# Optimization experiments

Measured on AMD Instinct MI355X. Metric: run time of the kernel, lower is better.

## Reference

```python
import jax, jax.numpy as jnp
import numpy as np

N_BUS = 300
N_GBUS = 69
N_LINE = 411
G_BUS0 = 1
VMAX = 1.06
VMIN = 0.94
L_LIMIT = 1.0
LG_MAX = (1.0, 1.0, 1.0)
BATCH = 32768


def setup_inputs() -> dict:
    key = jax.random.key(0)
    ks = jax.random.split(key, 18)
    f = lambda k, s: jax.random.normal(k, s, dtype=jnp.float32)
    return {
        "Volt": f(ks[0], (BATCH, 2 * N_BUS)),
        "P_Gens": f(ks[1], (BATCH, 2 * N_GBUS)),
        "P_Loads": f(ks[2], (BATCH, 2 * N_BUS)),
        "n_o_l_p": f(ks[3], (BATCH, 2 * N_BUS)),
        "n_o_mu_g_u": f(ks[4], (BATCH, 2 * N_GBUS)),
        "n_o_mu_g_d": f(ks[5], (BATCH, 2 * N_GBUS)),
        "n_o_mu_v_u": f(ks[6], (BATCH, N_BUS)),
        "n_o_mu_v_d": f(ks[7], (BATCH, N_BUS)),
        "n_o_mu_i_u": f(ks[8], (BATCH, N_LINE)),
        "Y": f(ks[9], (2 * N_BUS, 2 * N_BUS)) * 0.1,
        "Yconj": f(ks[10], (2 * N_BUS, 2 * N_BUS)) * 0.1,
        "Ybr": f(ks[11], (2 * N_LINE, 2 * N_LINE)) * 0.1,
        "IM": f(ks[12], (2 * N_LINE, 2 * N_BUS)) * 0.1,
        "Map_g": f(ks[13], (2 * N_GBUS, 2 * N_BUS)) * 0.1,
        "Map_L": f(ks[14], (2 * N_BUS, 2 * N_BUS)) * 0.1,
        "Gen_max": jax.random.uniform(ks[15], (1, 2 * N_GBUS), dtype=jnp.float32) + 0.5,
        "Gen_min": -jax.random.uniform(ks[16], (1, 2 * N_GBUS), dtype=jnp.float32) - 0.5,
        "C_Pg": f(ks[17], (1, N_GBUS)),
    }


def reference(Volt, P_Gens, P_Loads, n_o_l_p, n_o_mu_g_u, n_o_mu_g_d,
              n_o_mu_v_u, n_o_mu_v_d, n_o_mu_i_u,
              Y, Yconj, Ybr, IM, Map_g, Map_L, Gen_max, Gen_min, C_Pg):
    n = N_BUS
    B = Volt.shape[0]
    Bf = jnp.asarray(B, Volt.dtype)
    relu = jax.nn.relu

    Vre = Volt[:, :n]
    Vim = Volt[:, n:2 * n]

    # --- per-bus quadratic-form loop, vectorized ---------------------------
    # diag(Volt @ (M_i Y) @ Volt^T)[b] = Volt[b,i-1]*(Y[i-1]@Volt[b]) + Volt[b,n+i-1]*(Y[n+i-1]@Volt[b])
    quad_p = Volt * (Volt @ Y.T)      # [B, 2n]; quad_p[b,r] = Volt[b,r]*(Y[r]@Volt[b])
    quad_q = Volt * (Volt @ Yconj.T)  # [B, 2n]
    # TF broadcast quirk: [B] diag + [B,1] mismatch -> [B,B], reduce_sum(axis=1)
    # gives sum_j diag[j] (scalar) + B * mismatch[b].  Loop runs i = 1..n-1.
    scalar_pq = (jnp.sum(quad_p[:, 0:n - 1]) + jnp.sum(quad_p[:, n:2 * n - 1])
                 + jnp.sum(quad_q[:, 0:n - 1]) + jnp.sum(quad_q[:, n:2 * n - 1]))
    mism = P_Loads @ Map_L - P_Gens @ Map_g  # [B, 2n]
    mism_sum = jnp.sum(mism[:, 0:n - 1], axis=1) + jnp.sum(mism[:, n:2 * n - 1], axis=1)

    kkt = jnp.sum(jnp.abs(Volt[:, n + G_BUS0 - 1]))  # scalar seed
    kkt = kkt + scalar_pq + Bf * mism_sum            # -> [B]

    # --- inequality / complementarity terms --------------------------------
    kkt = kkt + jnp.sum(relu(P_Gens - Gen_max), axis=1)
    kkt = kkt + jnp.sum(relu(Gen_min - P_Gens), axis=1)

    v_up = Vre ** 2 + Vim ** 2 - VMAX ** 2
    v_dn = VMIN ** 2 - Vre ** 2 + Vim ** 2  # sign kept exactly as in original
    kkt = kkt + jnp.sum(relu(v_up), axis=1)
    kkt = kkt + jnp.sum(relu(v_dn), axis=1)

    Ibr = Volt @ IM.T @ Ybr.T  # == (Ybr @ (IM @ Volt^T))^T, [B, 2*n_line]
    i_up = Ibr[:, :N_LINE] ** 2 + Ibr[:, N_LINE:] ** 2 - L_LIMIT ** 2
    kkt = kkt + jnp.sum(relu(i_up), axis=1)

    kkt = kkt + jnp.sum(jnp.abs(n_o_mu_g_u * (P_Gens - Gen_max)), axis=1) / N_GBUS
    kkt = kkt + jnp.sum(jnp.abs(n_o_mu_g_d * (Gen_min - P_Gens)), axis=1) / N_GBUS
    kkt = kkt + jnp.sum(jnp.abs(n_o_mu_v_u * v_up), axis=1)
    kkt = kkt + jnp.sum(jnp.abs(n_o_mu_v_d * v_dn), axis=1)
    kkt = kkt + jnp.sum(jnp.abs(n_o_mu_i_u * i_up), axis=1)

    # --- stationarity w.r.t. generator injections ---------------------------
    C_Qg = jnp.zeros((1, N_GBUS), Volt.dtype)
    cost = jnp.concatenate([C_Pg, C_Qg], axis=1)  # [1, 2*n_gbus]
    stat = (n_o_mu_g_u * LG_MAX[1] - n_o_mu_g_d * LG_MAX[2]
            + (n_o_l_p * LG_MAX[0]) @ Map_g.T - cost)
    kkt = kkt + jnp.sum(jnp.abs(stat), axis=1)

    # --- dual feasibility ----------------------------------------------------
    kkt = kkt + jnp.sum(relu(-n_o_mu_g_u), axis=1)
    kkt = kkt + jnp.sum(relu(-n_o_mu_g_d), axis=1)
    kkt = kkt + jnp.sum(relu(-n_o_mu_v_u), axis=1)
    kkt = kkt + jnp.sum(relu(-n_o_mu_v_d), axis=1)
    kkt = kkt + jnp.sum(relu(-n_o_mu_i_u), axis=1)
    return kkt
```

## Files before the change

kernel.cpp:

```cpp
#include <hip/hip_runtime.h>

#define BATCH   32768
#define NLINE   411
#define NTILES  14
#define RTILES  256

typedef __attribute__((ext_vector_type(8))) short  short8;
typedef __attribute__((ext_vector_type(4))) float  f32x4;

#define WS_SCALAR   0
#define WS_KROWS    64
#define WS_MAPL     131136
#define WS_MAPG     133536
#define WS_ATMP     134144
#define WS_BMF      2106944
#define WS_VBF      4400704
#define WS_NEED_FAST (4400704 + 41943040)
#define WS_ZERO_BYTES 2106944

__device__ __forceinline__ unsigned short f2bf(float f) {
    unsigned int u = __float_as_uint(f);
    unsigned int r = (u + 0x7FFFu + ((u >> 16) & 1u)) >> 16;
    return (unsigned short)r;
}

#if defined(__has_builtin)
#  if __has_builtin(__builtin_amdgcn_cvt_pk_bf16_f32)
#    define HAVE_PK_BF16 1
#  endif
#endif

__device__ __forceinline__ unsigned int pk2bf(float a, float b) {
#ifdef HAVE_PK_BF16
    typedef __bf16 bf16x2 __attribute__((ext_vector_type(2)));
    bf16x2 r = __builtin_amdgcn_cvt_pk_bf16_f32(a, b);
    return __builtin_bit_cast(unsigned int, r);
#else
    return (unsigned int)f2bf(a) | ((unsigned int)f2bf(b) << 16);
#endif
}

__global__ void prep_colsums(const float* __restrict__ MapL, const float* __restrict__ Mapg,
                             float* __restrict__ mapL_s, float* __restrict__ mapg_s) {
    int w = threadIdx.x >> 6, lane = threadIdx.x & 63;
    int row = blockIdx.x * 4 + w;
    const float* src;
    float* dst;
    if (row < 600)      { src = MapL + (size_t)row * 600; dst = mapL_s + row; }
    else if (row < 738) { src = Mapg + (size_t)(row - 600) * 600; dst = mapg_s + (row - 600); }
    else return;
    float s = 0.f;
    for (int j = lane; j < 600; j += 64)
        if (j != 299 && j != 599) s += src[j];
    for (int m = 32; m >= 1; m >>= 1) s += __shfl_xor(s, m);
    if (lane == 0) *dst = s;
}

__global__ __launch_bounds__(256) void prep_A(const float* __restrict__ Ybr,
                                              const float* __restrict__ IM,
                                              float* __restrict__ Atmp) {
    int bid = blockIdx.x;
    int ks = bid & 3;
    int t2 = bid >> 2;
    int bc = t2 % 10, br = t2 / 10;
    int r0 = br * 64, c0 = bc * 64;
    int kb = ks * 206;
    int ke = (kb + 206 < 822) ? kb + 206 : 822;

    __shared__ float Yt[64][33];
    __shared__ float Xt[32][65];
    int t = threadIdx.x;
    int tx = t & 15, ty = t >> 4;
    float c[4][4] = {};

    for (int kk = kb; kk < ke; kk += 32) {
        __syncthreads();
        for (int e = t; e < 2048; e += 256) {
            int yr = e >> 5, yk = e & 31;
            int gr = r0 + yr, gk = kk + yk;
            Yt[yr][yk] = (gr < 822 && gk < ke) ? Ybr[(size_t)gr * 822 + gk] : 0.f;
        }
        for (int e = t; e < 2048; e += 256) {
            int xk = e >> 6, xc = e & 63;
            int gk = kk + xk, gc = c0 + xc;
            Xt[xk][xc] = (gk < ke && gc < 600) ? IM[(size_t)gk * 600 + gc] : 0.f;
        }
        __syncthreads();
        for (int k2 = 0; k2 < 32; ++k2) {
            float a[4], b[4];
#pragma unroll
            for (int ii = 0; ii < 4; ++ii) a[ii] = Yt[ty * 4 + ii][k2];
#pragma unroll
            for (int jj = 0; jj < 4; ++jj) b[jj] = Xt[k2][tx * 4 + jj];
#pragma unroll
            for (int ii = 0; ii < 4; ++ii)
#pragma unroll
                for (int jj = 0; jj < 4; ++jj) c[ii][jj] += a[ii] * b[jj];
        }
    }
#pragma unroll
    for (int ii = 0; ii < 4; ++ii)
#pragma unroll
        for (int jj = 0; jj < 4; ++jj) {
            int gr = r0 + ty * 4 + ii, gc = c0 + tx * 4 + jj;
            if (gr < 822 && gc < 600) atomicAdd(Atmp + (size_t)gr * 600 + gc, c[ii][jj]);
        }
}

__global__ void prep_packF(const float* __restrict__ Y, const float* __restrict__ Yconj,
                           const float* __restrict__ Mapg, const float* __restrict__ Atmp,
                           unsigned short* __restrict__ BmF) {
    int ntkc = blockIdx.x >> 2;
    int nt = ntkc / 10, kc = ntkc % 10;
    int S = (blockIdx.x & 3) * 256 + threadIdx.x;
    int ig = S >> 7, ks = (S >> 6) & 1, ln = S & 63;
    int rc = ig * 16 + (ln & 15);
    int kb = ks * 32 + ((ln >> 4) << 3);
    int n = nt * 128 + rc;
    unsigned short out[8];
#pragma unroll
    for (int j = 0; j < 8; ++j) {
        int k = kc * 64 + kb + j;
        float v = 0.f;
        if (k < 600) {
            if (n < 600) {
                if (n != 299 && n != 599)
                    v = Y[(size_t)n * 600 + k] + Yconj[(size_t)n * 600 + k];
            } else if (n >= 640 && n < 1536) {
                int idx = n - 640;
                int l = idx >> 1, h = idx & 1;
                if (l < NLINE) v = Atmp[(size_t)(h * NLINE + l) * 600 + k];
            } else if (n >= 1536) {
                int g = n - 1536;
                if (g < 138) v = Mapg[(size_t)g * 600 + k];
            }
        }
        out[j] = f2bf(v);
    }
    *(short8*)(BmF + (size_t)(ntkc * 1024 + S) * 8) = *(short8*)out;
}

__global__ __launch_bounds__(256) void prep_duties_conv(
    const float* __restrict__ Volt, const float* __restrict__ PL,
    const float* __restrict__ mu_vu, const float* __restrict__ mu_vd,
    const float* __restrict__ mapL_s, unsigned short* __restrict__ Vbf,
    float* __restrict__ kkt_rows, float* __restrict__ scalar_acc, int doConv) {
    __shared__ float mls[600];
    __shared__ float sred[4];
    int t = threadIdx.x;
    for (int j = t; j < 600; j += 256) mls[j] = mapL_s[j];
    __syncthreads();
    int w = t >> 6, lane = t & 63;
    int b = blockIdx.x * 4 + w;

    if (doConv) {
        for (int c = lane * 4; c < 600; c += 256) {
            f32x4 x = *(const f32x4*)(Volt + (size_t)b * 600 + c);
            uint2 p;
            p.x = pk2bf(x[0], x[1]);
            p.y = pk2bf(x[2], x[3]);
            *(uint2*)(Vbf + (size_t)b * 640 + c) = p;
        }
        if (lane < 10) {
            uint2 z = make_uint2(0u, 0u);
            *(uint2*)(Vbf + (size_t)b * 640 + 600 + lane * 4) = z;
        }
    }
    float s = 0.f;
    for (int j = lane; j < 300; j += 64) {
        float vr = Volt[(size_t)b * 600 + j];
        float vi = Volt[(size_t)b * 600 + 300 + j];
        float muu = mu_vu[(size_t)b * 300 + j];
        float mud = mu_vd[(size_t)b * 300 + j];
        float sq = vr * vr, si = vi * vi;
        float vu = sq + si - 1.1236f;
        float vd = 0.8836f - sq + si;
        s += fmaxf(vu, 0.f) + fmaxf(vd, 0.f) + fabsf(muu * vu) + fabsf(mud * vd)
           + fmaxf(-muu, 0.f) + fmaxf(-mud, 0.f);
    }
    float s2 = 0.f;
    for (int j = lane; j < 600; j += 64) s2 += PL[(size_t)b * 600 + j] * mls[j];
    s += 32768.0f * s2;
    for (int m = 32; m >= 1; m >>= 1) s += __shfl_xor(s, m);
    if (lane == 0) kkt_rows[b] = s;
    float v3 = (lane == 0) ? fabsf(Volt[(size_t)b * 600 + 300]) : 0.f;
    if (lane == 0) sred[w] = v3;
    __syncthreads();
    if (t == 0) atomicAdd(scalar_acc, sred[0] + sred[1] + sred[2] + sred[3]);
}

__global__ __launch_bounds__(256, 4) void kkt_main(
    const float* __restrict__ Volt, const float* __restrict__ nolp,
    const float* __restrict__ PG,
    const float* __restrict__ mu_gu, const float* __restrict__ mu_gd,
    const float* __restrict__ mu_iu,
    const float* __restrict__ Gmax, const float* __restrict__ Gmin,
    const float* __restrict__ CPg,
    const unsigned short* __restrict__ Vbf, const unsigned short* __restrict__ BmF,
    const float* __restrict__ mapg_s, float* __restrict__ kkt_rows,
    float* __restrict__ scalar_acc, int useVbf) {

    int idx = blockIdx.x;
    int xcd = idx & 7;
    int q = idx >> 3;
    int nt = q % NTILES;
    int rg = q / NTILES;
    int rt = rg * 8 + xcd;
    int b0 = rt * 128;

    int t = threadIdx.x;
    int lane = t & 63, w = t >> 6, wr = w >> 1, wc = w & 1;

    __shared__ short8 Asm[1024];
    __shared__ short8 Bsm[1024];
    __shared__ float  redbuf[4];

    bool fastA = (nt < 12) && useVbf;
    const float* Af32 = (nt < 12) ? Volt : nolp;

    int rcA[4], kbA[4];
#pragma unroll
    for (int m = 0; m < 4; ++m) {
        int S = m * 256 + t;
        int ig = S >> 7, ks = (S >> 6) & 1, ln = S & 63;
        rcA[m] = ig * 16 + (ln & 15);
        kbA[m] = ks * 32 + ((ln >> 4) << 3);
    }

    f32x4 acc[4][4] = {};

    for (int kc = 0; kc < 10; ++kc) {
        int k0 = kc * 64;
        __syncthreads();
        const unsigned short* bSrc = BmF + (size_t)(nt * 10 + kc) * 1024 * 8;
#pragma unroll
        for (int m = 0; m < 4; ++m) {
            int S = m * 256 + t;
            __builtin_amdgcn_global_load_lds(
                (const __attribute__((address_space(1))) unsigned int*)(bSrc + (size_t)S * 8),
                (__attribute__((address_space(3))) unsigned int*)&Bsm[S], 16, 0, 0);
        }
        if (fastA) {
#pragma unroll
            for (int m = 0; m < 4; ++m) {
                int S = m * 256 + t;
                __builtin_amdgcn_global_load_lds(
                    (const __attribute__((address_space(1))) unsigned int*)(Vbf + (size_t)(b0 + rcA[m]) * 640 + k0 + kbA[m]),
                    (__attribute__((address_space(3))) unsigned int*)&Asm[S], 16, 0, 0);
            }
        } else {
#pragma unroll
            for (int m = 0; m < 4; ++m) {
                int S = m * 256 + t;
                int gk = k0 + kbA[m];
                short8 av = (short8)0;
                if (gk < 600) {
                    const f32x4* p = (const f32x4*)(Af32 + (size_t)(b0 + rcA[m]) * 600 + gk);
                    f32x4 x0 = p[0], x1 = p[1];
                    uint2 a0, a1;
                    a0.x = pk2bf(x0[0], x0[1]); a0.y = pk2bf(x0[2], x0[3]);
                    a1.x = pk2bf(x1[0], x1[1]); a1.y = pk2bf(x1[2], x1[3]);
                    av = __builtin_bit_cast(short8, make_uint4(a0.x, a0.y, a1.x, a1.y));
                }
                Asm[S] = av;
            }
        }
        __syncthreads();
#pragma unroll
        for (int ks = 0; ks < 2; ++ks) {
            short8 af[4], bfr[4];
#pragma unroll
            for (int ii = 0; ii < 4; ++ii) af[ii] = Asm[((wr * 4 + ii) * 2 + ks) * 64 + lane];
#pragma unroll
            for (int jj = 0; jj < 4; ++jj) bfr[jj] = Bsm[((wc * 4 + jj) * 2 + ks) * 64 + lane];
#pragma unroll
            for (int ii = 0; ii < 4; ++ii)
#pragma unroll
                for (int jj = 0; jj < 4; ++jj)
                    acc[ii][jj] = __builtin_amdgcn_mfma_f32_16x16x32_bf16(af[ii], bfr[jj], acc[ii][jj], 0, 0, 0);
        }
    }

    if (nt < 5) {
        float qa = 0.f;
#pragma unroll
        for (int ii = 0; ii < 4; ++ii)
#pragma unroll
            for (int jj = 0; jj < 4; ++jj)
#pragma unroll
                for (int r2 = 0; r2 < 4; ++r2) {
                    int row = wr * 64 + ii * 16 + ((lane >> 4) << 2) + r2;
                    int col = nt * 128 + wc * 64 + jj * 16 + (lane & 15);
                    if (col < 600) {
                        float v = Volt[(size_t)(b0 + row) * 600 + col];
                        qa += acc[ii][jj][r2] * v;
                    }
                }
        for (int m = 32; m >= 1; m >>= 1) qa += __shfl_xor(qa, m);
        if (lane == 0) redbuf[w] = qa;
        __syncthreads();
        if (t == 0) atomicAdd(scalar_acc, redbuf[0] + redbuf[1] + redbuf[2] + redbuf[3]);
    } else if (nt < 12) {
        float racc[16];
#pragma unroll
        for (int s = 0; s < 16; ++s) racc[s] = 0.f;
#pragma unroll
        for (int ii = 0; ii < 4; ++ii)
#pragma unroll
            for (int jj = 0; jj < 4; ++jj)
#pragma unroll
                for (int r2 = 0; r2 < 4; ++r2) {
                    float u = acc[ii][jj][r2];
                    float up = __shfl_xor(u, 1);
                    int col = nt * 128 + wc * 64 + jj * 16 + (lane & 15);
                    int l = (col - 640) >> 1;
                    float contrib = 0.f;
                    if (l < NLINE && !(lane & 1)) {
                        int row = wr * 64 + ii * 16 + ((lane >> 4) << 2) + r2;
                        float iu = u * u + up * up - 1.0f;
                        float mu = mu_iu[(size_t)(b0 + row) * NLINE + l];
                        contrib = fmaxf(iu, 0.f) + fabsf(mu * iu) + fmaxf(-mu, 0.f);
                    }
                    racc[ii * 4 + r2] += contrib;
                }
#pragma unroll
        for (int s = 0; s < 16; ++s) {
            float v = racc[s];
            v += __shfl_xor(v, 1); v += __shfl_xor(v, 2);
            v += __shfl_xor(v, 4); v += __shfl_xor(v, 8);
            if ((lane & 15) == 0) {
                int row = wr * 64 + (s >> 2) * 16 + ((lane >> 4) << 2) + (s & 3);
                atomicAdd(kkt_rows + b0 + row, v);
            }
        }
    } else {
        float racc[16];
#pragma unroll
        for (int s = 0; s < 16; ++s) racc[s] = 0.f;
#pragma unroll
        for (int ii = 0; ii < 4; ++ii)
#pragma unroll
            for (int jj = 0; jj < 4; ++jj)
#pragma unroll
                for (int r2 = 0; r2 < 4; ++r2) {
                    int col = nt * 128 + wc * 64 + jj * 16 + (lane & 15);
                    int g = col - 1536;
                    float contrib = 0.f;
                    if (g < 138) {
                        int row = wr * 64 + ii * 16 + ((lane >> 4) << 2) + r2;
                        size_t ix = (size_t)(b0 + row) * 138 + g;
                        float u = acc[ii][jj][r2];
                        float gu = mu_gu[ix], gd = mu_gd[ix], pg = PG[ix];
                        float gmx = Gmax[g], gmn = Gmin[g];
                        float cst = (g < 69) ? CPg[g] : 0.f;
                        float t1 = pg - gmx, t2 = gmn - pg;
                        float st = u + gu - gd - cst;
                        contrib = fabsf(st) + fmaxf(t1, 0.f) + fmaxf(t2, 0.f)
                                + (fabsf(gu * t1) + fabsf(gd * t2)) * (1.0f / 69.0f)
                                + fmaxf(-gu, 0.f) + fmaxf(-gd, 0.f)
                                - 32768.0f * pg * mapg_s[g];
                    }
                    racc[ii * 4 + r2] += contrib;
                }
#pragma unroll
        for (int s = 0; s < 16; ++s) {
            float v = racc[s];
            v += __shfl_xor(v, 1); v += __shfl_xor(v, 2);
            v += __shfl_xor(v, 4); v += __shfl_xor(v, 8);
            if ((lane & 15) == 0) {
                int row = wr * 64 + (s >> 2) * 16 + ((lane >> 4) << 2) + (s & 3);
                atomicAdd(kkt_rows + b0 + row, v);
            }
        }
    }
}

__global__ void finalize_k(const float* __restrict__ kkt_rows, const float* __restrict__ scalar_acc,
                           float* __restrict__ out) {
    int i = blockIdx.x * 256 + threadIdx.x;
    out[i] = kkt_rows[i] + scalar_acc[0];
}

extern "C" void kernel_launch(void* const* d_in, const int* in_sizes, int n_in,
                              void* d_out, int out_size, void* d_ws, size_t ws_size,
                              hipStream_t stream) {
    const float* Volt  = (const float*)d_in[0];
    const float* PG    = (const float*)d_in[1];
    const float* PL    = (const float*)d_in[2];
    const float* nolp  = (const float*)d_in[3];
    const float* mu_gu = (const float*)d_in[4];
    const float* mu_gd = (const float*)d_in[5];
    const float* mu_vu = (const float*)d_in[6];
    const float* mu_vd = (const float*)d_in[7];
    const float* mu_iu = (const float*)d_in[8];
    const float* Y     = (const float*)d_in[9];
    const float* Yconj = (const float*)d_in[10];
    const float* Ybr   = (const float*)d_in[11];
    const float* IM    = (const float*)d_in[12];
    const float* Mapg  = (const float*)d_in[13];
    const float* MapL  = (const float*)d_in[14];
    const float* Gmax  = (const float*)d_in[15];
    const float* Gmin  = (const float*)d_in[16];
    const float* CPg   = (const float*)d_in[17];

    char* ws = (char*)d_ws;
    float* scalar_acc       = (float*)(ws + WS_SCALAR);
    float* kkt_rows         = (float*)(ws + WS_KROWS);
    float* mapLs            = (float*)(ws + WS_MAPL);
    float* mapgs            = (float*)(ws + WS_MAPG);
    float* Atmp             = (float*)(ws + WS_ATMP);
    unsigned short* BmF     = (unsigned short*)(ws + WS_BMF);
    unsigned short* Vbf     = (unsigned short*)(ws + WS_VBF);

    int useVbf = (ws_size >= (size_t)WS_NEED_FAST) ? 1 : 0;

    hipMemsetAsync(d_ws, 0, WS_ZERO_BYTES, stream);
    prep_colsums<<<185, 256, 0, stream>>>(MapL, Mapg, mapLs, mapgs);
    prep_A<<<520, 256, 0, stream>>>(Ybr, IM, Atmp);
    prep_packF<<<560, 256, 0, stream>>>(Y, Yconj, Mapg, Atmp, BmF);
    prep_duties_conv<<<8192, 256, 0, stream>>>(Volt, PL, mu_vu, mu_vd, mapLs,
                                               Vbf, kkt_rows, scalar_acc, useVbf);
    kkt_main<<<RTILES * NTILES, 256, 0, stream>>>(Volt, nolp, PG, mu_gu, mu_gd, mu_iu,
                                                  Gmax, Gmin, CPg, Vbf, BmF, mapgs,
                                                  kkt_rows, scalar_acc, useVbf);
    finalize_k<<<BATCH / 256, 256, 0, stream>>>(kkt_rows, scalar_acc, (float*)d_out);
}
```

Before: 789.0 us.

## Fuse prep into persistent row-block GEMM with A resident in LDS

Each 64-row block now converts its Volt (and later nolp) slab to bf16 once into LDS and sweeps all 14 column tiles, double-buffering B tiles via async global-to-LDS loads. The separate Volt-to-bf16 conversion kernel and the bf16 workspace copy are removed, and the per-row duty and load terms are folded into the first iterations of the main loop. This cuts repeated global reads of A across column tiles and one kernel launch. The cost is a large LDS footprint and one block per CU (512 blocks), so there is less latency hiding.

```diff
diff --git a/kernel.cpp b/kernel.cpp
--- a/kernel.cpp
+++ b/kernel.cpp
@@ -3,7 +3,9 @@
 #define BATCH   32768
 #define NLINE   411
 #define NTILES  14
-#define RTILES  256
+#define PAIRS   7
+#define ROWS    64
+#define NBLK    (BATCH / ROWS)
 
 typedef __attribute__((ext_vector_type(8))) short  short8;
 typedef __attribute__((ext_vector_type(4))) float  f32x4;
@@ -14,8 +16,6 @@
 #define WS_MAPG     133536
 #define WS_ATMP     134144
 #define WS_BMF      2106944
-#define WS_VBF      4400704
-#define WS_NEED_FAST (4400704 + 41943040)
 #define WS_ZERO_BYTES 2106944
 
 __device__ __forceinline__ unsigned short f2bf(float f) {
@@ -140,239 +140,244 @@
     *(short8*)(BmF + (size_t)(ntkc * 1024 + S) * 8) = *(short8*)out;
 }
 
-__global__ __launch_bounds__(256) void prep_duties_conv(
-    const float* __restrict__ Volt, const float* __restrict__ PL,
+__device__ __forceinline__ void stage_a(const float* __restrict__ src, int b0,
+                                        short8* Abuf, int t) {
+#pragma unroll
+    for (int h = 0; h < 2; ++h) {
+        f32x4 x[20];
+        int Sb = h * 2560;
+#pragma unroll
+        for (int m = 0; m < 10; ++m) {
+            int S = Sb + m * 256 + t;
+            int kc = S >> 9, r = S & 511;
+            int g = r >> 6, ln = r & 63;
+            int row = b0 + ((g >> 1) << 4) + (ln & 15);
+            int k = (kc << 6) + ((g & 1) << 5) + ((ln >> 4) << 3);
+            if (k < 600) {
+                const f32x4* p = (const f32x4*)(src + (size_t)row * 600 + k);
+                x[2 * m] = p[0]; x[2 * m + 1] = p[1];
+            } else {
+                f32x4 z = {0.f, 0.f, 0.f, 0.f};
+                x[2 * m] = z; x[2 * m + 1] = z;
+            }
+        }
+#pragma unroll
+        for (int m = 0; m < 10; ++m) {
+            int S = Sb + m * 256 + t;
+            f32x4 a = x[2 * m], b = x[2 * m + 1];
+            Abuf[S] = __builtin_bit_cast(short8,
+                make_uint4(pk2bf(a[0], a[1]), pk2bf(a[2], a[3]),
+                           pk2bf(b[0], b[1]), pk2bf(b[2], b[3])));
+        }
+    }
+}
+
+__device__ __forceinline__ void issue_b(const unsigned short* __restrict__ BmF,
+                                        int p, int kc, short8* dst, int t) {
+#pragma unroll
+    for (int m = 0; m < 8; ++m) {
+        int S = m * 256 + t;
+        int ntl2 = S >> 10, Sl = S & 1023;
+        const unsigned short* src = BmF +
+            (size_t)(((p * 2 + ntl2) * 10 + kc) * 1024 + Sl) * 8;
+        __builtin_amdgcn_global_load_lds(
+            (const __attribute__((address_space(1))) unsigned int*)src,
+            (__attribute__((address_space(3))) unsigned int*)(dst + S), 16, 0, 0);
+    }
+}
+
+__global__ __launch_bounds__(256, 1) void kkt_main(
+    const float* __restrict__ Volt, const float* __restrict__ nolp,
+    const float* __restrict__ PG, const float* __restrict__ PL,
+    const float* __restrict__ mu_gu, const float* __restrict__ mu_gd,
     const float* __restrict__ mu_vu, const float* __restrict__ mu_vd,
-    const float* __restrict__ mapL_s, unsigned short* __restrict__ Vbf,
-    float* __restrict__ kkt_rows, float* __restrict__ scalar_acc, int doConv) {
-    __shared__ float mls[600];
-    __shared__ float sred[4];
-    int t = threadIdx.x;
-    for (int j = t; j < 600; j += 256) mls[j] = mapL_s[j];
-    __syncthreads();
-    int w = t >> 6, lane = t & 63;
-    int b = blockIdx.x * 4 + w;
-
-    if (doConv) {
-        for (int c = lane * 4; c < 600; c += 256) {
-            f32x4 x = *(const f32x4*)(Volt + (size_t)b * 600 + c);
-            uint2 p;
-            p.x = pk2bf(x[0], x[1]);
-            p.y = pk2bf(x[2], x[3]);
-            *(uint2*)(Vbf + (size_t)b * 640 + c) = p;
-        }
-        if (lane < 10) {
-            uint2 z = make_uint2(0u, 0u);
-            *(uint2*)(Vbf + (size_t)b * 640 + 600 + lane * 4) = z;
-        }
-    }
-    float s = 0.f;
-    for (int j = lane; j < 300; j += 64) {
-        float vr = Volt[(size_t)b * 600 + j];
-        float vi = Volt[(size_t)b * 600 + 300 + j];
-        float muu = mu_vu[(size_t)b * 300 + j];
-        float mud = mu_vd[(size_t)b * 300 + j];
-        float sq = vr * vr, si = vi * vi;
-        float vu = sq + si - 1.1236f;
-        float vd = 0.8836f - sq + si;
-        s += fmaxf(vu, 0.f) + fmaxf(vd, 0.f) + fabsf(muu * vu) + fabsf(mud * vd)
-           + fmaxf(-muu, 0.f) + fmaxf(-mud, 0.f);
-    }
-    float s2 = 0.f;
-    for (int j = lane; j < 600; j += 64) s2 += PL[(size_t)b * 600 + j] * mls[j];
-    s += 32768.0f * s2;
-    for (int m = 32; m >= 1; m >>= 1) s += __shfl_xor(s, m);
-    if (lane == 0) kkt_rows[b] = s;
-    float v3 = (lane == 0) ? fabsf(Volt[(size_t)b * 600 + 300]) : 0.f;
-    if (lane == 0) sred[w] = v3;
-    __syncthreads();
-    if (t == 0) atomicAdd(scalar_acc, sred[0] + sred[1] + sred[2] + sred[3]);
-}
-
-__global__ __launch_bounds__(256, 4) void kkt_main(
-    const float* __restrict__ Volt, const float* __restrict__ nolp,
-    const float* __restrict__ PG,
-    const float* __restrict__ mu_gu, const float* __restrict__ mu_gd,
     const float* __restrict__ mu_iu,
     const float* __restrict__ Gmax, const float* __restrict__ Gmin,
     const float* __restrict__ CPg,
-    const unsigned short* __restrict__ Vbf, const unsigned short* __restrict__ BmF,
-    const float* __restrict__ mapg_s, float* __restrict__ kkt_rows,
-    float* __restrict__ scalar_acc, int useVbf) {
-
-    int idx = blockIdx.x;
-    int xcd = idx & 7;
-    int q = idx >> 3;
-    int nt = q % NTILES;
-    int rg = q / NTILES;
-    int rt = rg * 8 + xcd;
-    int b0 = rt * 128;
-
-    int t = threadIdx.x;
-    int lane = t & 63, w = t >> 6, wr = w >> 1, wc = w & 1;
-
-    __shared__ short8 Asm[1024];
-    __shared__ short8 Bsm[1024];
-    __shared__ float  redbuf[4];
-
-    bool fastA = (nt < 12) && useVbf;
-    const float* Af32 = (nt < 12) ? Volt : nolp;
-
-    int rcA[4], kbA[4];
-#pragma unroll
-    for (int m = 0; m < 4; ++m) {
-        int S = m * 256 + t;
-        int ig = S >> 7, ks = (S >> 6) & 1, ln = S & 63;
-        rcA[m] = ig * 16 + (ln & 15);
-        kbA[m] = ks * 32 + ((ln >> 4) << 3);
-    }
+    const unsigned short* __restrict__ BmF,
+    const float* __restrict__ mapLs, const float* __restrict__ mapgs,
+    float* __restrict__ kkt_rows, float* __restrict__ scalar_acc) {
+
+    __shared__ short8 Abuf[5120];
+    __shared__ short8 Bsm[2][2048];
+    __shared__ float  mls[600];
+    __shared__ float  sacc;
+
+    int t = threadIdx.x, lane = t & 63, w = t >> 6;
+    int b0 = blockIdx.x * ROWS;
+    int ntl = w >> 1, wc2 = w & 1;
+
+    if (t == 0) sacc = 0.f;
+    for (int j = t; j < 600; j += 256) mls[j] = mapLs[j];
+
+    stage_a(Volt, b0, Abuf, t);
+    issue_b(BmF, 0, 0, &Bsm[0][0], t);
+    __syncthreads();
 
     f32x4 acc[4][4] = {};
-
-    for (int kc = 0; kc < 10; ++kc) {
-        int k0 = kc * 64;
-        __syncthreads();
-        const unsigned short* bSrc = BmF + (size_t)(nt * 10 + kc) * 1024 * 8;
-#pragma unroll
-        for (int m = 0; m < 4; ++m) {
-            int S = m * 256 + t;
-            __builtin_amdgcn_global_load_lds(
-                (const __attribute__((address_space(1))) unsigned int*)(bSrc + (size_t)S * 8),
-                (__attribute__((address_space(3))) unsigned int*)&Bsm[S], 16, 0, 0);
-        }
-        if (fastA) {
-#pragma unroll
-            for (int m = 0; m < 4; ++m) {
-                int S = m * 256 + t;
-                __builtin_amdgcn_global_load_lds(
-                    (const __attribute__((address_space(1))) unsigned int*)(Vbf + (size_t)(b0 + rcA[m]) * 640 + k0 + kbA[m]),
-                    (__attribute__((address_space(3))) unsigned int*)&Asm[S], 16, 0, 0);
-            }
-        } else {
-#pragma unroll
-            for (int m = 0; m < 4; ++m) {
-                int S = m * 256 + t;
-                int gk = k0 + kbA[m];
-                short8 av = (short8)0;
-                if (gk < 600) {
-                    const f32x4* p = (const f32x4*)(Af32 + (size_t)(b0 + rcA[m]) * 600 + gk);
-                    f32x4 x0 = p[0], x1 = p[1];
-                    uint2 a0, a1;
-                    a0.x = pk2bf(x0[0], x0[1]); a0.y = pk2bf(x0[2], x0[3]);
-                    a1.x = pk2bf(x1[0], x1[1]); a1.y = pk2bf(x1[2], x1[3]);
-                    av = __builtin_bit_cast(short8, make_uint4(a0.x, a0.y, a1.x, a1.y));
-                }
-                Asm[S] = av;
-            }
-        }
-        __syncthreads();
+    float dscal = 0.f;
+
+    for (int s = 0; s < PAIRS * 10; ++s) {
+        int p = s / 10, kc = s % 10;
+
+        if (s == 60) {
+            stage_a(nolp, b0, Abuf, t);
+            __syncthreads();
+        }
+        int sn = s + 1;
+        if (sn < PAIRS * 10) issue_b(BmF, sn / 10, sn % 10, &Bsm[sn & 1][0], t);
+
+        const short8* Ak = Abuf + kc * 512;
+        const short8* Bp = &Bsm[s & 1][ntl * 1024];
 #pragma unroll
         for (int ks = 0; ks < 2; ++ks) {
             short8 af[4], bfr[4];
 #pragma unroll
-            for (int ii = 0; ii < 4; ++ii) af[ii] = Asm[((wr * 4 + ii) * 2 + ks) * 64 + lane];
-#pragma unroll
-            for (int jj = 0; jj < 4; ++jj) bfr[jj] = Bsm[((wc * 4 + jj) * 2 + ks) * 64 + lane];
+            for (int ii = 0; ii < 4; ++ii) af[ii] = Ak[(((ii << 1) | ks) << 6) + lane];
+#pragma unroll
+            for (int jj = 0; jj < 4; ++jj)
+                bfr[jj] = Bp[(((((wc2 << 2) | jj) << 1) | ks) << 6) + lane];
 #pragma unroll
             for (int ii = 0; ii < 4; ++ii)
 #pragma unroll
                 for (int jj = 0; jj < 4; ++jj)
                     acc[ii][jj] = __builtin_amdgcn_mfma_f32_16x16x32_bf16(af[ii], bfr[jj], acc[ii][jj], 0, 0, 0);
         }
-    }
-
-    if (nt < 5) {
-        float qa = 0.f;
-#pragma unroll
-        for (int ii = 0; ii < 4; ++ii)
-#pragma unroll
-            for (int jj = 0; jj < 4; ++jj)
-#pragma unroll
-                for (int r2 = 0; r2 < 4; ++r2) {
-                    int row = wr * 64 + ii * 16 + ((lane >> 4) << 2) + r2;
-                    int col = nt * 128 + wc * 64 + jj * 16 + (lane & 15);
-                    if (col < 600) {
-                        float v = Volt[(size_t)(b0 + row) * 600 + col];
-                        qa += acc[ii][jj][r2] * v;
+
+        if (s < 16) {
+            int r = b0 + s * 4 + w;
+            const float* vrow = Volt + (size_t)r * 600;
+            float sd = 0.f;
+            for (int j = lane; j < 300; j += 64) {
+                float vr = vrow[j], vi = vrow[300 + j];
+                float muu = mu_vu[(size_t)r * 300 + j];
+                float mud = mu_vd[(size_t)r * 300 + j];
+                float sq = vr * vr, si = vi * vi;
+                float vu = sq + si - 1.1236f;
+                float vd = 0.8836f - sq + si;
+                sd += fmaxf(vu, 0.f) + fmaxf(vd, 0.f) + fabsf(muu * vu) + fabsf(mud * vd)
+                    + fmaxf(-muu, 0.f) + fmaxf(-mud, 0.f);
+            }
+            float s2 = 0.f;
+            for (int j = lane; j < 600; j += 64) s2 += PL[(size_t)r * 600 + j] * mls[j];
+            sd += 32768.0f * s2;
+            for (int m = 32; m >= 1; m >>= 1) sd += __shfl_xor(sd, m);
+            if (lane == 0) {
+                atomicAdd(kkt_rows + r, sd);
+                dscal += fabsf(vrow[300]);
+            }
+        }
+
+        if (kc == 9) {
+            int cb = p * 4 + w;
+            int c0 = cb * 64;
+            if (cb < 10) {
+                float qa = 0.f;
+#pragma unroll
+                for (int ii = 0; ii < 4; ++ii)
+#pragma unroll
+                    for (int jj = 0; jj < 4; ++jj) {
+                        int col = c0 + jj * 16 + (lane & 15);
+                        if (col < 600) {
+#pragma unroll
+                            for (int r2 = 0; r2 < 4; ++r2) {
+                                int row = ii * 16 + ((lane >> 4) << 2) + r2;
+                                qa += acc[ii][jj][r2] * Volt[(size_t)(b0 + row) * 600 + col];
+                            }
+                        }
+                    }
+                for (int m = 32; m >= 1; m >>= 1) qa += __shfl_xor(qa, m);
+                if (lane == 0) atomicAdd(&sacc, qa);
+            } else if (cb < 24) {
+                float racc[16];
+#pragma unroll
+                for (int q2 = 0; q2 < 16; ++q2) racc[q2] = 0.f;
+#pragma unroll
+                for (int ii = 0; ii < 4; ++ii)
+#pragma unroll
+                    for (int jj = 0; jj < 4; ++jj) {
+                        int col = c0 + jj * 16 + (lane & 15);
+                        int l = (col - 640) >> 1;
+#pragma unroll
+                        for (int r2 = 0; r2 < 4; ++r2) {
+                            float u = acc[ii][jj][r2];
+                            float up = __shfl_xor(u, 1);
+                            float contrib = 0.f;
+                            if (l < NLINE && !(lane & 1)) {
+                                int row = ii * 16 + ((lane >> 4) << 2) + r2;
+                                float iu = u * u + up * up - 1.0f;
+                                float mu = mu_iu[(size_t)(b0 + row) * NLINE + l];
+                                contrib = fmaxf(iu, 0.f) + fabsf(mu * iu) + fmaxf(-mu, 0.f);
+                            }
+                            racc[ii * 4 + r2] += contrib;
+                        }
+                    }
+#pragma unroll
+                for (int q2 = 0; q2 < 16; ++q2) {
+                    float v = racc[q2];
+                    v += __shfl_xor(v, 1); v += __shfl_xor(v, 2);
+                    v += __shfl_xor(v, 4); v += __shfl_xor(v, 8);
+                    if ((lane & 15) == 0) {
+                        int row = (q2 >> 2) * 16 + ((lane >> 4) << 2) + (q2 & 3);
+                        atomicAdd(kkt_rows + b0 + row, v);
                     }
                 }
-        for (int m = 32; m >= 1; m >>= 1) qa += __shfl_xor(qa, m);
-        if (lane == 0) redbuf[w] = qa;
+            } else {
+                float racc[16];
+#pragma unroll
+                for (int q2 = 0; q2 < 16; ++q2) racc[q2] = 0.f;
+#pragma unroll
+                for (int ii = 0; ii < 4; ++ii)
+#pragma unroll
+                    for (int jj = 0; jj < 4; ++jj) {
+                        int col = c0 + jj * 16 + (lane & 15);
+                        int g = col - 1536;
+#pragma unroll
+                        for (int r2 = 0; r2 < 4; ++r2) {
+                            float contrib = 0.f;
+                            if (g < 138) {
+                                int row = ii * 16 + ((lane >> 4) << 2) + r2;
+                                size_t ix = (size_t)(b0 + row) * 138 + g;
+                                float u = acc[ii][jj][r2];
+                                float gu = mu_gu[ix], gd = mu_gd[ix], pg = PG[ix];
+                                float gmx = Gmax[g], gmn = Gmin[g];
+                                float cst = (g < 69) ? CPg[g] : 0.f;
+                                float t1 = pg - gmx, t2 = gmn - pg;
+                                float st = u + gu - gd - cst;
+                                contrib = fabsf(st) + fmaxf(t1, 0.f) + fmaxf(t2, 0.f)
+                                        + (fabsf(gu * t1) + fabsf(gd * t2)) * (1.0f / 69.0f)
+                                        + fmaxf(-gu, 0.f) + fmaxf(-gd, 0.f)
+                                        - 32768.0f * pg * mapgs[g];
+                            }
+                            racc[ii * 4 + r2] += contrib;
+                        }
+                    }
+#pragma unroll
+                for (int q2 = 0; q2 < 16; ++q2) {
+                    float v = racc[q2];
+                    v += __shfl_xor(v, 1); v += __shfl_xor(v, 2);
+                    v += __shfl_xor(v, 4); v += __shfl_xor(v, 8);
+                    if ((lane & 15) == 0) {
+                        int row = (q2 >> 2) * 16 + ((lane >> 4) << 2) + (q2 & 3);
+                        atomicAdd(kkt_rows + b0 + row, v);
+                    }
+                }
+            }
+#pragma unroll
+            for (int ii = 0; ii < 4; ++ii)
+#pragma unroll
+                for (int jj = 0; jj < 4; ++jj) {
+                    f32x4 z = {0.f, 0.f, 0.f, 0.f};
+                    acc[ii][jj] = z;
+                }
+        }
+
         __syncthreads();
-        if (t == 0) atomicAdd(scalar_acc, redbuf[0] + redbuf[1] + redbuf[2] + redbuf[3]);
-    } else if (nt < 12) {
-        float racc[16];
-#pragma unroll
-        for (int s = 0; s < 16; ++s) racc[s] = 0.f;
-#pragma unroll
-        for (int ii = 0; ii < 4; ++ii)
-#pragma unroll
-            for (int jj = 0; jj < 4; ++jj)
-#pragma unroll
-                for (int r2 = 0; r2 < 4; ++r2) {
-                    float u = acc[ii][jj][r2];
-                    float up = __shfl_xor(u, 1);
-                    int col = nt * 128 + wc * 64 + jj * 16 + (lane & 15);
-                    int l = (col - 640) >> 1;
-                    float contrib = 0.f;
-                    if (l < NLINE && !(lane & 1)) {
-                        int row = wr * 64 + ii * 16 + ((lane >> 4) << 2) + r2;
-                        float iu = u * u + up * up - 1.0f;
-                        float mu = mu_iu[(size_t)(b0 + row) * NLINE + l];
-                        contrib = fmaxf(iu, 0.f) + fabsf(mu * iu) + fmaxf(-mu, 0.f);
-                    }
-                    racc[ii * 4 + r2] += contrib;
-                }
-#pragma unroll
-        for (int s = 0; s < 16; ++s) {
-            float v = racc[s];
-            v += __shfl_xor(v, 1); v += __shfl_xor(v, 2);
-            v += __shfl_xor(v, 4); v += __shfl_xor(v, 8);
-            if ((lane & 15) == 0) {
-                int row = wr * 64 + (s >> 2) * 16 + ((lane >> 4) << 2) + (s & 3);
-                atomicAdd(kkt_rows + b0 + row, v);
-            }
-        }
-    } else {
-        float racc[16];
-#pragma unroll
-        for (int s = 0; s < 16; ++s) racc[s] = 0.f;
-#pragma unroll
-        for (int ii = 0; ii < 4; ++ii)
-#pragma unroll
-            for (int jj = 0; jj < 4; ++jj)
-#pragma unroll
-                for (int r2 = 0; r2 < 4; ++r2) {
-                    int col = nt * 128 + wc * 64 + jj * 16 + (lane & 15);
-                    int g = col - 1536;
-                    float contrib = 0.f;
-                    if (g < 138) {
-                        int row = wr * 64 + ii * 16 + ((lane >> 4) << 2) + r2;
-                        size_t ix = (size_t)(b0 + row) * 138 + g;
-                        float u = acc[ii][jj][r2];
-                        float gu = mu_gu[ix], gd = mu_gd[ix], pg = PG[ix];
-                        float gmx = Gmax[g], gmn = Gmin[g];
-                        float cst = (g < 69) ? CPg[g] : 0.f;
-                        float t1 = pg - gmx, t2 = gmn - pg;
-                        float st = u + gu - gd - cst;
-                        contrib = fabsf(st) + fmaxf(t1, 0.f) + fmaxf(t2, 0.f)
-                                + (fabsf(gu * t1) + fabsf(gd * t2)) * (1.0f / 69.0f)
-                                + fmaxf(-gu, 0.f) + fmaxf(-gd, 0.f)
-                                - 32768.0f * pg * mapg_s[g];
-                    }
-                    racc[ii * 4 + r2] += contrib;
-                }
-#pragma unroll
-        for (int s = 0; s < 16; ++s) {
-            float v = racc[s];
-            v += __shfl_xor(v, 1); v += __shfl_xor(v, 2);
-            v += __shfl_xor(v, 4); v += __shfl_xor(v, 8);
-            if ((lane & 15) == 0) {
-                int row = wr * 64 + (s >> 2) * 16 + ((lane >> 4) << 2) + (s & 3);
-                atomicAdd(kkt_rows + b0 + row, v);
-            }
-        }
     }
+
+    if (lane == 0) atomicAdd(&sacc, dscal);
+    __syncthreads();
+    if (t == 0) atomicAdd(scalar_acc, sacc);
 }
 
 __global__ void finalize_k(const float* __restrict__ kkt_rows, const float* __restrict__ scalar_acc,
@@ -410,18 +415,13 @@
     float* mapgs            = (float*)(ws + WS_MAPG);
     float* Atmp             = (float*)(ws + WS_ATMP);
     unsigned short* BmF     = (unsigned short*)(ws + WS_BMF);
-    unsigned short* Vbf     = (unsigned short*)(ws + WS_VBF);
-
-    int useVbf = (ws_size >= (size_t)WS_NEED_FAST) ? 1 : 0;
 
     hipMemsetAsync(d_ws, 0, WS_ZERO_BYTES, stream);
     prep_colsums<<<185, 256, 0, stream>>>(MapL, Mapg, mapLs, mapgs);
     prep_A<<<520, 256, 0, stream>>>(Ybr, IM, Atmp);
     prep_packF<<<560, 256, 0, stream>>>(Y, Yconj, Mapg, Atmp, BmF);
-    prep_duties_conv<<<8192, 256, 0, stream>>>(Volt, PL, mu_vu, mu_vd, mapLs,
-                                               Vbf, kkt_rows, scalar_acc, useVbf);
-    kkt_main<<<RTILES * NTILES, 256, 0, stream>>>(Volt, nolp, PG, mu_gu, mu_gd, mu_iu,
-                                                  Gmax, Gmin, CPg, Vbf, BmF, mapgs,
-                                                  kkt_rows, scalar_acc, useVbf);
+    kkt_main<<<NBLK, 256, 0, stream>>>(Volt, nolp, PG, PL, mu_gu, mu_gd, mu_vu, mu_vd,
+                                       mu_iu, Gmax, Gmin, CPg, BmF, mapLs, mapgs,
+                                       kkt_rows, scalar_acc);
     finalize_k<<<BATCH / 256, 256, 0, stream>>>(kkt_rows, scalar_acc, (float*)d_out);
 }
```

New measurement: 1.085 ms. 37.5% more time.

## Double-buffer GEMM tiles and fold per-row duty terms into main kernel

Applied to the files above, without the earlier changes.

Merges the column-sum, B-packing and Volt-to-bf16 prep kernels into one launch. Moves the per-row voltage duty and load-map terms into the GEMM kernel, distributed across n-tiles and interleaved with the k-loop. Adds LDS double buffering so the next k-chunk's loads overlap the current MFMA work. This costs twice the LDS tiles and lowers the launch-bounds occupancy hint, and it adds extra atomics on row accumulators.

```diff
diff --git a/kernel.cpp b/kernel.cpp
--- a/kernel.cpp
+++ b/kernel.cpp
@@ -38,22 +38,6 @@
 #else
     return (unsigned int)f2bf(a) | ((unsigned int)f2bf(b) << 16);
 #endif
-}
-
-__global__ void prep_colsums(const float* __restrict__ MapL, const float* __restrict__ Mapg,
-                             float* __restrict__ mapL_s, float* __restrict__ mapg_s) {
-    int w = threadIdx.x >> 6, lane = threadIdx.x & 63;
-    int row = blockIdx.x * 4 + w;
-    const float* src;
-    float* dst;
-    if (row < 600)      { src = MapL + (size_t)row * 600; dst = mapL_s + row; }
-    else if (row < 738) { src = Mapg + (size_t)(row - 600) * 600; dst = mapg_s + (row - 600); }
-    else return;
-    float s = 0.f;
-    for (int j = lane; j < 600; j += 64)
-        if (j != 299 && j != 599) s += src[j];
-    for (int m = 32; m >= 1; m >>= 1) s += __shfl_xor(s, m);
-    if (lane == 0) *dst = s;
 }
 
 __global__ __launch_bounds__(256) void prep_A(const float* __restrict__ Ybr,
@@ -107,53 +91,61 @@
         }
 }
 
-__global__ void prep_packF(const float* __restrict__ Y, const float* __restrict__ Yconj,
-                           const float* __restrict__ Mapg, const float* __restrict__ Atmp,
-                           unsigned short* __restrict__ BmF) {
-    int ntkc = blockIdx.x >> 2;
-    int nt = ntkc / 10, kc = ntkc % 10;
-    int S = (blockIdx.x & 3) * 256 + threadIdx.x;
-    int ig = S >> 7, ks = (S >> 6) & 1, ln = S & 63;
-    int rc = ig * 16 + (ln & 15);
-    int kb = ks * 32 + ((ln >> 4) << 3);
-    int n = nt * 128 + rc;
-    unsigned short out[8];
-#pragma unroll
-    for (int j = 0; j < 8; ++j) {
-        int k = kc * 64 + kb + j;
-        float v = 0.f;
-        if (k < 600) {
-            if (n < 600) {
-                if (n != 299 && n != 599)
-                    v = Y[(size_t)n * 600 + k] + Yconj[(size_t)n * 600 + k];
-            } else if (n >= 640 && n < 1536) {
-                int idx = n - 640;
-                int l = idx >> 1, h = idx & 1;
-                if (l < NLINE) v = Atmp[(size_t)(h * NLINE + l) * 600 + k];
-            } else if (n >= 1536) {
-                int g = n - 1536;
-                if (g < 138) v = Mapg[(size_t)g * 600 + k];
+__global__ __launch_bounds__(256) void prep_misc(
+    const float* __restrict__ MapL, const float* __restrict__ Mapg,
+    float* __restrict__ mapL_s, float* __restrict__ mapg_s,
+    const float* __restrict__ Y, const float* __restrict__ Yconj,
+    const float* __restrict__ Atmp, unsigned short* __restrict__ BmF,
+    const float* __restrict__ Volt, unsigned short* __restrict__ Vbf, int doConv) {
+    int bid = blockIdx.x;
+    int t = threadIdx.x;
+    int w = t >> 6, lane = t & 63;
+
+    if (bid < 185) {
+        int row = bid * 4 + w;
+        const float* src;
+        float* dst;
+        if (row < 600)      { src = MapL + (size_t)row * 600; dst = mapL_s + row; }
+        else if (row < 738) { src = Mapg + (size_t)(row - 600) * 600; dst = mapg_s + (row - 600); }
+        else return;
+        float s = 0.f;
+        for (int j = lane; j < 600; j += 64)
+            if (j != 299 && j != 599) s += src[j];
+        for (int m = 32; m >= 1; m >>= 1) s += __shfl_xor(s, m);
+        if (lane == 0) *dst = s;
+    } else if (bid < 745) {
+        int b2 = bid - 185;
+        int ntkc = b2 >> 2;
+        int nt = ntkc / 10, kc = ntkc % 10;
+        int S = (b2 & 3) * 256 + t;
+        int ig = S >> 7, ks = (S >> 6) & 1, ln = S & 63;
+        int rc = ig * 16 + (ln & 15);
+        int kb = ks * 32 + ((ln >> 4) << 3);
+        int n = nt * 128 + rc;
+        unsigned short out[8];
+#pragma unroll
+        for (int j = 0; j < 8; ++j) {
+            int k = kc * 64 + kb + j;
+            float v = 0.f;
+            if (k < 600) {
+                if (n < 600) {
+                    if (n != 299 && n != 599)
+                        v = Y[(size_t)n * 600 + k] + Yconj[(size_t)n * 600 + k];
+                } else if (n >= 640 && n < 1536) {
+                    int idx = n - 640;
+                    int l = idx >> 1, h = idx & 1;
+                    if (l < NLINE) v = Atmp[(size_t)(h * NLINE + l) * 600 + k];
+                } else if (n >= 1536) {
+                    int g = n - 1536;
+                    if (g < 138) v = Mapg[(size_t)g * 600 + k];
+                }
             }
-        }
-        out[j] = f2bf(v);
-    }
-    *(short8*)(BmF + (size_t)(ntkc * 1024 + S) * 8) = *(short8*)out;
-}
-
-__global__ __launch_bounds__(256) void prep_duties_conv(
-    const float* __restrict__ Volt, const float* __restrict__ PL,
-    const float* __restrict__ mu_vu, const float* __restrict__ mu_vd,
-    const float* __restrict__ mapL_s, unsigned short* __restrict__ Vbf,
-    float* __restrict__ kkt_rows, float* __restrict__ scalar_acc, int doConv) {
-    __shared__ float mls[600];
-    __shared__ float sred[4];
-    int t = threadIdx.x;
-    for (int j = t; j < 600; j += 256) mls[j] = mapL_s[j];
-    __syncthreads();
-    int w = t >> 6, lane = t & 63;
-    int b = blockIdx.x * 4 + w;
-
-    if (doConv) {
+            out[j] = f2bf(v);
+        }
+        *(short8*)(BmF + (size_t)(ntkc * 1024 + S) * 8) = *(short8*)out;
+    } else {
+        if (!doConv) return;
+        int b = (bid - 745) * 4 + w;
         for (int c = lane * 4; c < 600; c += 256) {
             f32x4 x = *(const f32x4*)(Volt + (size_t)b * 600 + c);
             uint2 p;
@@ -166,39 +158,19 @@
             *(uint2*)(Vbf + (size_t)b * 640 + 600 + lane * 4) = z;
         }
     }
-    float s = 0.f;
-    for (int j = lane; j < 300; j += 64) {
-        float vr = Volt[(size_t)b * 600 + j];
-        float vi = Volt[(size_t)b * 600 + 300 + j];
-        float muu = mu_vu[(size_t)b * 300 + j];
-        float mud = mu_vd[(size_t)b * 300 + j];
-        float sq = vr * vr, si = vi * vi;
-        float vu = sq + si - 1.1236f;
-        float vd = 0.8836f - sq + si;
-        s += fmaxf(vu, 0.f) + fmaxf(vd, 0.f) + fabsf(muu * vu) + fabsf(mud * vd)
-           + fmaxf(-muu, 0.f) + fmaxf(-mud, 0.f);
-    }
-    float s2 = 0.f;
-    for (int j = lane; j < 600; j += 64) s2 += PL[(size_t)b * 600 + j] * mls[j];
-    s += 32768.0f * s2;
-    for (int m = 32; m >= 1; m >>= 1) s += __shfl_xor(s, m);
-    if (lane == 0) kkt_rows[b] = s;
-    float v3 = (lane == 0) ? fabsf(Volt[(size_t)b * 600 + 300]) : 0.f;
-    if (lane == 0) sred[w] = v3;
-    __syncthreads();
-    if (t == 0) atomicAdd(scalar_acc, sred[0] + sred[1] + sred[2] + sred[3]);
-}
-
-__global__ __launch_bounds__(256, 4) void kkt_main(
+}
+
+__global__ __launch_bounds__(256, 2) void kkt_main(
     const float* __restrict__ Volt, const float* __restrict__ nolp,
-    const float* __restrict__ PG,
+    const float* __restrict__ PG, const float* __restrict__ PL,
     const float* __restrict__ mu_gu, const float* __restrict__ mu_gd,
+    const float* __restrict__ mu_vu, const float* __restrict__ mu_vd,
     const float* __restrict__ mu_iu,
     const float* __restrict__ Gmax, const float* __restrict__ Gmin,
     const float* __restrict__ CPg,
     const unsigned short* __restrict__ Vbf, const unsigned short* __restrict__ BmF,
-    const float* __restrict__ mapg_s, float* __restrict__ kkt_rows,
-    float* __restrict__ scalar_acc, int useVbf) {
+    const float* __restrict__ mapLs, const float* __restrict__ mapgs,
+    float* __restrict__ kkt_rows, float* __restrict__ scalar_acc, int useVbf) {
 
     int idx = blockIdx.x;
     int xcd = idx & 7;
@@ -211,12 +183,15 @@
     int t = threadIdx.x;
     int lane = t & 63, w = t >> 6, wr = w >> 1, wc = w & 1;
 
-    __shared__ short8 Asm[1024];
-    __shared__ short8 Bsm[1024];
+    __shared__ short8 Asm[2][1024];
+    __shared__ short8 Bsm[2][1024];
+    __shared__ float  mls[600];
     __shared__ float  redbuf[4];
 
     bool fastA = (nt < 12) && useVbf;
     const float* Af32 = (nt < 12) ? Volt : nolp;
+
+    for (int j = t; j < 600; j += 256) mls[j] = mapLs[j];
 
     int rcA[4], kbA[4];
 #pragma unroll
@@ -227,59 +202,128 @@
         kbA[m] = ks * 32 + ((ln >> 4) << 3);
     }
 
-    f32x4 acc[4][4] = {};
-
-    for (int kc = 0; kc < 10; ++kc) {
-        int k0 = kc * 64;
-        __syncthreads();
-        const unsigned short* bSrc = BmF + (size_t)(nt * 10 + kc) * 1024 * 8;
+    auto issueB = [&](int kc, int pb) {
+        const unsigned short* bSrc = BmF + (size_t)(nt * 10 + kc) * 8192;
 #pragma unroll
         for (int m = 0; m < 4; ++m) {
             int S = m * 256 + t;
             __builtin_amdgcn_global_load_lds(
                 (const __attribute__((address_space(1))) unsigned int*)(bSrc + (size_t)S * 8),
-                (__attribute__((address_space(3))) unsigned int*)&Bsm[S], 16, 0, 0);
-        }
-        if (fastA) {
-#pragma unroll
-            for (int m = 0; m < 4; ++m) {
-                int S = m * 256 + t;
-                __builtin_amdgcn_global_load_lds(
-                    (const __attribute__((address_space(1))) unsigned int*)(Vbf + (size_t)(b0 + rcA[m]) * 640 + k0 + kbA[m]),
-                    (__attribute__((address_space(3))) unsigned int*)&Asm[S], 16, 0, 0);
+                (__attribute__((address_space(3))) unsigned int*)&Bsm[pb][S], 16, 0, 0);
+        }
+    };
+    auto issueA = [&](int kc, int pb) {
+#pragma unroll
+        for (int m = 0; m < 4; ++m) {
+            int S = m * 256 + t;
+            __builtin_amdgcn_global_load_lds(
+                (const __attribute__((address_space(1))) unsigned int*)(Vbf + (size_t)(b0 + rcA[m]) * 640 + kc * 64 + kbA[m]),
+                (__attribute__((address_space(3))) unsigned int*)&Asm[pb][S], 16, 0, 0);
+        }
+    };
+    auto loadA = [&](int kc, f32x4* xa) {
+#pragma unroll
+        for (int m = 0; m < 4; ++m) {
+            int gk = kc * 64 + kbA[m];
+            if (gk < 600) {
+                const f32x4* p = (const f32x4*)(Af32 + (size_t)(b0 + rcA[m]) * 600 + gk);
+                xa[2 * m] = p[0]; xa[2 * m + 1] = p[1];
+            } else {
+                f32x4 z = {0.f, 0.f, 0.f, 0.f};
+                xa[2 * m] = z; xa[2 * m + 1] = z;
             }
-        } else {
-#pragma unroll
-            for (int m = 0; m < 4; ++m) {
-                int S = m * 256 + t;
-                int gk = k0 + kbA[m];
-                short8 av = (short8)0;
-                if (gk < 600) {
-                    const f32x4* p = (const f32x4*)(Af32 + (size_t)(b0 + rcA[m]) * 600 + gk);
-                    f32x4 x0 = p[0], x1 = p[1];
-                    uint2 a0, a1;
-                    a0.x = pk2bf(x0[0], x0[1]); a0.y = pk2bf(x0[2], x0[3]);
-                    a1.x = pk2bf(x1[0], x1[1]); a1.y = pk2bf(x1[2], x1[3]);
-                    av = __builtin_bit_cast(short8, make_uint4(a0.x, a0.y, a1.x, a1.y));
-                }
-                Asm[S] = av;
-            }
-        }
-        __syncthreads();
+        }
+    };
+    auto writeA = [&](const f32x4* xa, int pb) {
+#pragma unroll
+        for (int m = 0; m < 4; ++m) {
+            int S = m * 256 + t;
+            f32x4 a = xa[2 * m], b = xa[2 * m + 1];
+            Asm[pb][S] = __builtin_bit_cast(short8,
+                make_uint4(pk2bf(a[0], a[1]), pk2bf(a[2], a[3]),
+                           pk2bf(b[0], b[1]), pk2bf(b[2], b[3])));
+        }
+    };
+
+    issueB(0, 0);
+    if (fastA) issueA(0, 0);
+    else { f32x4 x0[8]; loadA(0, x0); writeA(x0, 0); }
+    __syncthreads();
+
+    f32x4 acc[4][4] = {};
+    float dscal = 0.f;
+    int cur = 0;
+
+    for (int kc = 0; kc < 10; ++kc) {
+        int nxt = cur ^ 1;
+        bool havN = (kc < 9);
+        f32x4 xa[8];
+        if (havN) {
+            issueB(kc + 1, nxt);
+            if (fastA) issueA(kc + 1, nxt);
+            else       loadA(kc + 1, xa);
+        }
+
+        const short8* Ak = Asm[cur];
+        const short8* Bk = Bsm[cur];
 #pragma unroll
         for (int ks = 0; ks < 2; ++ks) {
             short8 af[4], bfr[4];
 #pragma unroll
-            for (int ii = 0; ii < 4; ++ii) af[ii] = Asm[((wr * 4 + ii) * 2 + ks) * 64 + lane];
-#pragma unroll
-            for (int jj = 0; jj < 4; ++jj) bfr[jj] = Bsm[((wc * 4 + jj) * 2 + ks) * 64 + lane];
+            for (int ii = 0; ii < 4; ++ii) af[ii] = Ak[((wr * 4 + ii) * 2 + ks) * 64 + lane];
+#pragma unroll
+            for (int jj = 0; jj < 4; ++jj) bfr[jj] = Bk[((wc * 4 + jj) * 2 + ks) * 64 + lane];
 #pragma unroll
             for (int ii = 0; ii < 4; ++ii)
 #pragma unroll
                 for (int jj = 0; jj < 4; ++jj)
                     acc[ii][jj] = __builtin_amdgcn_mfma_f32_16x16x32_bf16(af[ii], bfr[jj], acc[ii][jj], 0, 0, 0);
         }
+
+        if (kc < 3) {
+            int i = kc * 4 + w;
+            int rl = nt + 14 * i;
+            if (i < 10 && rl < 128) {
+                int r = b0 + rl;
+                const float* vrow = Volt + (size_t)r * 600;
+                float sd = 0.f;
+                for (int j = lane * 4; j < 300; j += 256) {
+                    f32x4 vr  = *(const f32x4*)(vrow + j);
+                    f32x4 vi  = *(const f32x4*)(vrow + 300 + j);
+                    f32x4 muu = *(const f32x4*)(mu_vu + (size_t)r * 300 + j);
+                    f32x4 mud = *(const f32x4*)(mu_vd + (size_t)r * 300 + j);
+#pragma unroll
+                    for (int e = 0; e < 4; ++e) {
+                        float sq = vr[e] * vr[e], si = vi[e] * vi[e];
+                        float vu = sq + si - 1.1236f;
+                        float vd = 0.8836f - sq + si;
+                        sd += fmaxf(vu, 0.f) + fmaxf(vd, 0.f)
+                            + fabsf(muu[e] * vu) + fabsf(mud[e] * vd)
+                            + fmaxf(-muu[e], 0.f) + fmaxf(-mud[e], 0.f);
+                    }
+                }
+                float s2 = 0.f;
+                for (int j = lane * 4; j < 600; j += 256) {
+                    f32x4 pl = *(const f32x4*)(PL + (size_t)r * 600 + j);
+#pragma unroll
+                    for (int e = 0; e < 4; ++e) s2 += pl[e] * mls[j + e];
+                }
+                sd += 32768.0f * s2;
+                for (int m = 32; m >= 1; m >>= 1) sd += __shfl_xor(sd, m);
+                if (lane == 0) {
+                    atomicAdd(kkt_rows + r, sd);
+                    dscal += fabsf(vrow[300]);
+                }
+            }
+        }
+
+        if (havN && !fastA) writeA(xa, nxt);
+
+        __syncthreads();
+        cur = nxt;
     }
+
+    if (lane == 0 && dscal != 0.f) atomicAdd(scalar_acc, dscal);
 
     if (nt < 5) {
         float qa = 0.f;
@@ -358,7 +402,7 @@
                         contrib = fabsf(st) + fmaxf(t1, 0.f) + fmaxf(t2, 0.f)
                                 + (fabsf(gu * t1) + fabsf(gd * t2)) * (1.0f / 69.0f)
                                 + fmaxf(-gu, 0.f) + fmaxf(-gd, 0.f)
-                                - 32768.0f * pg * mapg_s[g];
+                                - 32768.0f * pg * mapgs[g];
                     }
                     racc[ii * 4 + r2] += contrib;
                 }
@@ -415,13 +459,12 @@
     int useVbf = (ws_size >= (size_t)WS_NEED_FAST) ? 1 : 0;
 
     hipMemsetAsync(d_ws, 0, WS_ZERO_BYTES, stream);
-    prep_colsums<<<185, 256, 0, stream>>>(MapL, Mapg, mapLs, mapgs);
     prep_A<<<520, 256, 0, stream>>>(Ybr, IM, Atmp);
-    prep_packF<<<560, 256, 0, stream>>>(Y, Yconj, Mapg, Atmp, BmF);
-    prep_duties_conv<<<8192, 256, 0, stream>>>(Volt, PL, mu_vu, mu_vd, mapLs,
-                                               Vbf, kkt_rows, scalar_acc, useVbf);
-    kkt_main<<<RTILES * NTILES, 256, 0, stream>>>(Volt, nolp, PG, mu_gu, mu_gd, mu_iu,
-                                                  Gmax, Gmin, CPg, Vbf, BmF, mapgs,
+    prep_misc<<<185 + 560 + 8192, 256, 0, stream>>>(MapL, Mapg, mapLs, mapgs,
+                                                    Y, Yconj, Atmp, BmF, Volt, Vbf, useVbf);
+    kkt_main<<<RTILES * NTILES, 256, 0, stream>>>(Volt, nolp, PG, PL, mu_gu, mu_gd,
+                                                  mu_vu, mu_vd, mu_iu, Gmax, Gmin, CPg,
+                                                  Vbf, BmF, mapLs, mapgs,
                                                   kkt_rows, scalar_acc, useVbf);
     finalize_k<<<BATCH / 256, 256, 0, stream>>>(kkt_rows, scalar_acc, (float*)d_out);
 }
```

Measured after the change: 816.7 us. 1.04x slower.
